# Kernel optimization log

Hardware: AMD Instinct MI355X
Metric: run time of the kernel (lower is better)

The kernel has to match this reference:

```python
import jax, jax.numpy as jnp
import numpy as np

H = 128
W = 128
TILE = 32
N = 12000
BIG = 1e30


def _render(means2D, cov2d, color, opacity, depths):
    # pixel coords, indexing='xy': pix[y, x] = (x, y)
    pix = jnp.stack(jnp.meshgrid(jnp.arange(W), jnp.arange(H), indexing='xy'), axis=-1).astype(means2D.dtype)
    c00 = cov2d[:, 0, 0]; c01 = cov2d[:, 0, 1]; c10 = cov2d[:, 1, 0]; c11 = cov2d[:, 1, 1]
    det = c00 * c11 - c01 * c10
    # get_radius (no_grad in torch)
    mid = 0.5 * (c00 + c11)
    s = jnp.sqrt(jnp.maximum(mid * mid - det, 0.1))
    radii = jax.lax.stop_gradient(3.0 * jnp.ceil(jnp.sqrt(jnp.maximum(mid + s, mid - s))))
    # get_rect, clipped to image bounds
    rmin = jnp.clip(means2D - radii[:, None], 0.0, W - 1.0)  # H == W == 128
    rmax = jnp.clip(means2D + radii[:, None], 0.0, W - 1.0)
    rmin = jax.lax.stop_gradient(rmin)
    rmax = jax.lax.stop_gradient(rmax)
    # closed-form 2x2 inverse (conic)
    inv_det = 1.0 / det
    conic = jnp.stack([jnp.stack([c11, -c01], axis=-1),
                       jnp.stack([-c10, c00], axis=-1)], axis=-2) * inv_det[:, None, None]

    img_c = jnp.ones((H, W, 3), means2D.dtype)
    img_d = jnp.zeros((H, W, 1), means2D.dtype)
    img_a = jnp.zeros((H, W, 1), means2D.dtype)

    for h in range(0, H, TILE):
        for w in range(0, W, TILE):
            tlx = jnp.maximum(rmin[:, 0], w); tly = jnp.maximum(rmin[:, 1], h)
            brx = jnp.minimum(rmax[:, 0], w + TILE - 1.0); bry = jnp.minimum(rmax[:, 1], h + TILE - 1.0)
            mask = (brx > tlx) & (bry > tly)  # [N]
            # depth sort with non-intersecting gaussians pushed to the back
            order = jnp.argsort(jnp.where(mask, depths, BIG))
            sm = means2D[order]          # [N,2]
            sc = conic[order]            # [N,2,2]
            so = opacity[order]          # [N,1]
            scol = color[order]          # [N,3]
            smask = mask[order]
            sd = jnp.where(smask, depths[order], 0.0)
            tile_coord = pix[h:h + TILE, w:w + TILE].reshape(-1, 2)  # [1024,2]
            dx = tile_coord[:, None, :] - sm[None]                   # [1024,N,2]
            gw = jnp.exp(-0.5 * (dx[..., 0] ** 2 * sc[:, 0, 0]
                                 + dx[..., 1] ** 2 * sc[:, 1, 1]
                                 + dx[..., 0] * dx[..., 1] * (sc[:, 0, 1] + sc[:, 1, 0])))
            alpha = gw[..., None] * so[None] * smask[None, :, None].astype(gw.dtype)  # [1024,N,1]
            alpha = jnp.minimum(alpha, 0.99)
            T = jnp.cumprod(jnp.concatenate([jnp.ones_like(alpha[:, :1]), 1.0 - alpha[:, :-1]], axis=1), axis=1)
            wgt = T * alpha
            acc = wgt.sum(axis=1)                                   # [1024,1]
            tc = (wgt * scol[None]).sum(axis=1) + (1.0 - acc)       # white background
            td = (wgt * sd[None, :, None]).sum(axis=1)
            img_c = img_c.at[h:h + TILE, w:w + TILE].set(tc.reshape(TILE, TILE, 3))
            img_d = img_d.at[h:h + TILE, w:w + TILE].set(td.reshape(TILE, TILE, 1))
            img_a = img_a.at[h:h + TILE, w:w + TILE].set(acc.reshape(TILE, TILE, 1))
    return img_c, img_d, img_a


def setup_inputs() -> dict:
    key = jax.random.key(0)
    k1, k2, k3, k4, k5 = jax.random.split(key, 5)
    means2D = jax.random.uniform(k1, (N, 2), jnp.float32) * 128.0
    L = 0.6 * jax.random.normal(k2, (N, 2, 2), jnp.float32)
    cov2d = L @ jnp.swapaxes(L, -1, -2) + 0.3 * jnp.eye(2, dtype=jnp.float32)[None]
    color = jax.random.uniform(k3, (N, 3), jnp.float32)
    opacity = jax.random.uniform(k4, (N, 1), jnp.float32)
    depths = jax.random.uniform(k5, (N,), jnp.float32) * 10.0 + 0.2
    return {"means2D": means2D, "cov2d": cov2d, "color": color, "opacity": opacity, "depths": depths}


def reference(means2D, cov2d, color, opacity, depths):
    return _render(means2D, cov2d, color, opacity, depths)
```

## Files before the change

### kernel.cpp

```cpp
#include <hip/hip_runtime.h>
#include <stdint.h>

#define HH 128
#define WW 128
#define NTILES 16
#define NPIX (HH * WW)
#define MAXSEG 16
#define JCH 512

__device__ __forceinline__ uint64_t mkkey(float d, int i) {
    return ((uint64_t)__float_as_uint(d) << 32) | (uint64_t)(uint32_t)i;
}

__global__ __launch_bounds__(256) void k1_rank(const float* __restrict__ depths,
                                               int* __restrict__ part,
                                               int N, int ncj, int NA) {
    int bi = blockIdx.x / ncj;
    int bj = blockIdx.x % ncj;
    int t  = threadIdx.x;
    int i  = bi * 256 + t;
    float di = (i < N) ? depths[i] : 0.0f;
    uint64_t ki = mkkey(di, i);

    int j0   = bj * JCH;
    int jend = min(N, j0 + JCH);

    int c0 = 0, c1 = 0, c2 = 0, c3 = 0;
    int j = j0;
    for (; j + 4 <= jend; j += 4) {
        uint64_t a = mkkey(depths[j + 0], j + 0);
        uint64_t b = mkkey(depths[j + 1], j + 1);
        uint64_t c = mkkey(depths[j + 2], j + 2);
        uint64_t d = mkkey(depths[j + 3], j + 3);
        c0 += (a < ki);
        c1 += (b < ki);
        c2 += (c < ki);
        c3 += (d < ki);
    }
    for (; j < jend; j++) c0 += (mkkey(depths[j], j) < ki);

    if (i < N) part[(size_t)bj * NA + i] = (c0 + c1) + (c2 + c3);
}

__global__ __launch_bounds__(256) void k2_scatter(const float* __restrict__ means,
                                                  const float* __restrict__ cov,
                                                  const float* __restrict__ color,
                                                  const float* __restrict__ opac,
                                                  const float* __restrict__ depths,
                                                  const int* __restrict__ part,
                                                  float* __restrict__ sorted,
                                                  int* __restrict__ smask,
                                                  int N, int ncj, int NA) {
    int i = blockIdx.x * blockDim.x + threadIdx.x;
    if (i >= N) return;

    int r = 0;
    for (int b = 0; b < ncj; b++) r += part[(size_t)b * NA + i];

    float mx = means[2 * i + 0];
    float my = means[2 * i + 1];
    float c00 = cov[4 * i + 0];
    float c01 = cov[4 * i + 1];
    float c10 = cov[4 * i + 2];
    float c11 = cov[4 * i + 3];

    float det = c00 * c11 - c01 * c10;
    float mid = 0.5f * (c00 + c11);
    float s = sqrtf(fmaxf(mid * mid - det, 0.1f));
    float radii = 3.0f * ceilf(sqrtf(fmaxf(mid + s, mid - s)));

    float rminx = fminf(fmaxf(mx - radii, 0.0f), (float)(WW - 1));
    float rminy = fminf(fmaxf(my - radii, 0.0f), (float)(HH - 1));
    float rmaxx = fminf(fmaxf(mx + radii, 0.0f), (float)(WW - 1));
    float rmaxy = fminf(fmaxf(my + radii, 0.0f), (float)(HH - 1));

    float inv_det = 1.0f / det;
    float A = c11 * inv_det;
    float B = c00 * inv_det;
    float C = -(c01 + c10) * inv_det;

    int bits = 0;
    for (int ty = 0; ty < 4; ty++) {
        float h = (float)(ty * 32);
        float tly = fmaxf(rminy, h);
        float bry = fminf(rmaxy, h + 31.0f);
        bool yok = bry > tly;
        for (int tx = 0; tx < 4; tx++) {
            float w = (float)(tx * 32);
            float tlx = fmaxf(rminx, w);
            float brx = fminf(rmaxx, w + 31.0f);
            if (yok && (brx > tlx)) bits |= 1 << (ty * 4 + tx);
        }
    }

    float4* g4 = (float4*)(sorted + (size_t)r * 12);
    g4[0] = make_float4(mx, my, A, B);
    g4[1] = make_float4(C, opac[i], color[3 * i + 0], color[3 * i + 1]);
    g4[2] = make_float4(color[3 * i + 2], depths[i], 0.0f, 0.0f);
    smask[r] = bits;
}

__global__ __launch_bounds__(1024) void k3_compact(const int* __restrict__ smask,
                                                   int* __restrict__ lists,
                                                   int* __restrict__ counts,
                                                   int N) {
    int tile = blockIdx.x;
    int t = threadIdx.x;
    int lane = t & 63;
    int wv = t >> 6;

    __shared__ int wsum[16];
    __shared__ int woff[16];
    __shared__ int s_run;
    if (t == 0) s_run = 0;
    __syncthreads();

    int* list = lists + (size_t)tile * N;

    for (int base = 0; base < N; base += 1024) {
        int idx = base + t;
        int flag = (idx < N) ? ((smask[idx] >> tile) & 1) : 0;
        unsigned long long bal = __ballot(flag);
        int pre = __popcll(bal & ((1ull << lane) - 1ull));
        if (lane == 63) wsum[wv] = pre + flag;
        __syncthreads();
        if (wv == 0 && lane < 16) {
            int v = 0;
            for (int q = 0; q < lane; q++) v += wsum[q];
            woff[lane] = v;
        }
        __syncthreads();
        int run = s_run;
        if (flag) list[run + woff[wv] + pre] = idx;
        __syncthreads();
        if (t == 0) s_run = run + woff[15] + wsum[15];
        __syncthreads();
    }
    if (t == 0) counts[tile] = s_run;
}

#define CH 64
__global__ __launch_bounds__(256) void k4_render(const float* __restrict__ sorted,
                                                 const int* __restrict__ lists,
                                                 const int* __restrict__ counts,
                                                 float4* __restrict__ part4,
                                                 float2* __restrict__ part2,
                                                 int N, int S) {
    int b = blockIdx.x;
    int s = b & (S - 1);
    int q = b / S;
    int tile = q >> 2;
    int sub = q & 3;
    int tx = tile & 3;
    int ty = tile >> 2;
    int t = threadIdx.x;

    int p = sub * 256 + t;
    int px = p & 31;
    int py = p >> 5;
    float fx = (float)(tx * 32 + px);
    float fy = (float)(ty * 32 + py);

    int cnt = counts[tile];
    int chunk = (cnt + S - 1) / S;
    int beg = s * chunk;
    int end = min(cnt, beg + chunk);
    const int* list = lists + (size_t)tile * N;

    __shared__ __align__(16) float4 s_g[CH * 3];
    __shared__ int s_idx[CH];

    float T = 1.0f;
    float ar = 0.0f, ag = 0.0f, ab = 0.0f, ad = 0.0f, aa = 0.0f;

    for (int base = beg; base < end; base += CH) {
        int m = min(CH, end - base);
        if (t < CH) s_idx[t] = (t < m) ? list[base + t] : 0;
        __syncthreads();
        if (t < m * 3) {
            int k = t / 3;
            int c = t - k * 3;
            s_g[t] = ((const float4*)(sorted + (size_t)s_idx[k] * 12))[c];
        }
        __syncthreads();
        for (int k = 0; k < m; k++) {
            float4 ga = s_g[k * 3 + 0];
            float4 gb = s_g[k * 3 + 1];
            float4 gc = s_g[k * 3 + 2];
            float dx = fx - ga.x;
            float dy = fy - ga.y;
            float e = ga.z * dx * dx + ga.w * dy * dy + gb.x * dx * dy;
            float gw = __expf(-0.5f * e);
            float alpha = fminf(gw * gb.y, 0.99f);
            float w = T * alpha;
            ar += w * gb.z;
            ag += w * gb.w;
            ab += w * gc.x;
            ad += w * gc.y;
            aa += w;
            T *= (1.0f - alpha);
        }
        __syncthreads();
    }

    size_t o = (size_t)s * NPIX + (size_t)tile * 1024 + p;
    part4[o] = make_float4(ar, ag, ab, ad);
    part2[o] = make_float2(aa, T);
}

__global__ __launch_bounds__(256) void k5_combine(const float4* __restrict__ part4,
                                                  const float2* __restrict__ part2,
                                                  float* __restrict__ out, int S) {
    int pid = blockIdx.x * 256 + threadIdx.x;
    int tile = pid >> 10;
    int p = pid & 1023;
    int px = p & 31;
    int py = p >> 5;
    int gx = (tile & 3) * 32 + px;
    int gy = (tile >> 2) * 32 + py;

    float T = 1.0f;
    float ar = 0.0f, ag = 0.0f, ab = 0.0f, ad = 0.0f, aa = 0.0f;
    for (int s = 0; s < S; s++) {
        float4 q4 = part4[(size_t)s * NPIX + pid];
        float2 q2 = part2[(size_t)s * NPIX + pid];
        ar += T * q4.x;
        ag += T * q4.y;
        ab += T * q4.z;
        ad += T * q4.w;
        aa += T * q2.x;
        T *= q2.y;
    }

    int pidx = gy * WW + gx;
    float bgr = 1.0f - aa;
    out[pidx * 3 + 0] = ar + bgr;
    out[pidx * 3 + 1] = ag + bgr;
    out[pidx * 3 + 2] = ab + bgr;
    out[HH * WW * 3 + pidx] = ad;
    out[HH * WW * 4 + pidx] = aa;
}

extern "C" void kernel_launch(void* const* d_in, const int* in_sizes, int n_in,
                              void* d_out, int out_size, void* d_ws, size_t ws_size,
                              hipStream_t stream) {
    const float* means  = (const float*)d_in[0];
    const float* cov    = (const float*)d_in[1];
    const float* color  = (const float*)d_in[2];
    const float* opac   = (const float*)d_in[3];
    const float* depths = (const float*)d_in[4];
    float* out = (float*)d_out;

    int N = in_sizes[4];
    int NA = (int)(((size_t)N + 255) / 256 * 256);
    int nb  = (N + 255) / 256;
    int ncj = (N + JCH - 1) / JCH;

    size_t o_part   = 0;
    size_t o_sorted = o_part + (size_t)ncj * NA * 4;
    size_t o_smask  = o_sorted + (size_t)NA * 48;
    size_t o_lists  = o_smask + (size_t)NA * 4;
    size_t o_counts = o_lists + (size_t)NTILES * NA * 4;
    size_t o_part4  = o_counts + 256;

    int S = 1;
    while (S < MAXSEG &&
           o_part4 + (size_t)(S * 2) * NPIX * 24 <= ws_size) S *= 2;
    size_t o_part2 = o_part4 + (size_t)S * NPIX * 16;

    int*    part   = (int*)((char*)d_ws + o_part);
    float*  sorted = (float*)((char*)d_ws + o_sorted);
    int*    smask  = (int*)((char*)d_ws + o_smask);
    int*    lists  = (int*)((char*)d_ws + o_lists);
    int*    counts = (int*)((char*)d_ws + o_counts);
    float4* part4  = (float4*)((char*)d_ws + o_part4);
    float2* part2  = (float2*)((char*)d_ws + o_part2);

    k1_rank<<<nb * ncj, 256, 0, stream>>>(depths, part, N, ncj, NA);
    k2_scatter<<<nb, 256, 0, stream>>>(means, cov, color, opac, depths, part,
                                       sorted, smask, N, ncj, NA);
    k3_compact<<<NTILES, 1024, 0, stream>>>(smask, lists, counts, N);
    k4_render<<<64 * S, 256, 0, stream>>>(sorted, lists, counts, part4, part2,
                                          N, S);
    k5_combine<<<NPIX / 256, 256, 0, stream>>>(part4, part2, out, S);
}
```

Baseline: 140.1 us.

## Fuse rank with scatter and compaction with render into two kernels

Cuts the pipeline from five kernels to two. Rank counting and the scatter now share one block: four wave slices each count over a quarter of the keys and reduce through shared memory. Per-tile compaction is merged with rendering, keeping the tile list in LDS, and one 1024-thread block per tile renders all pixels with no segment split or combine pass. This removes launch overhead and global intermediates but leaves only 16 blocks for the heavy render, cutting parallelism sharply, and the list is capped at LCAP entries.

```diff
diff --git a/kernel.cpp b/kernel.cpp
--- a/kernel.cpp
+++ b/kernel.cpp
@@ -4,118 +4,108 @@
 #define HH 128
 #define WW 128
 #define NTILES 16
-#define NPIX (HH * WW)
-#define MAXSEG 16
-#define JCH 512
+#define LCAP 12288
+#define CH 128
 
 __device__ __forceinline__ uint64_t mkkey(float d, int i) {
     return ((uint64_t)__float_as_uint(d) << 32) | (uint64_t)(uint32_t)i;
 }
 
-__global__ __launch_bounds__(256) void k1_rank(const float* __restrict__ depths,
-                                               int* __restrict__ part,
-                                               int N, int ncj, int NA) {
-    int bi = blockIdx.x / ncj;
-    int bj = blockIdx.x % ncj;
-    int t  = threadIdx.x;
-    int i  = bi * 256 + t;
+__global__ __launch_bounds__(256) void kA(const float* __restrict__ means,
+                                          const float* __restrict__ cov,
+                                          const float* __restrict__ color,
+                                          const float* __restrict__ opac,
+                                          const float* __restrict__ depths,
+                                          float* __restrict__ sorted,
+                                          int* __restrict__ smask, int N) {
+    int t = threadIdx.x;
+    int slice = t >> 6;
+    int il = t & 63;
+    int i = blockIdx.x * 64 + il;
     float di = (i < N) ? depths[i] : 0.0f;
     uint64_t ki = mkkey(di, i);
 
-    int j0   = bj * JCH;
-    int jend = min(N, j0 + JCH);
+    int per = (N + 3) / 4;
+    int j0 = slice * per;
+    int jend = min(N, j0 + per);
 
     int c0 = 0, c1 = 0, c2 = 0, c3 = 0;
     int j = j0;
     for (; j + 4 <= jend; j += 4) {
-        uint64_t a = mkkey(depths[j + 0], j + 0);
-        uint64_t b = mkkey(depths[j + 1], j + 1);
-        uint64_t c = mkkey(depths[j + 2], j + 2);
-        uint64_t d = mkkey(depths[j + 3], j + 3);
-        c0 += (a < ki);
-        c1 += (b < ki);
-        c2 += (c < ki);
-        c3 += (d < ki);
+        c0 += (mkkey(depths[j + 0], j + 0) < ki);
+        c1 += (mkkey(depths[j + 1], j + 1) < ki);
+        c2 += (mkkey(depths[j + 2], j + 2) < ki);
+        c3 += (mkkey(depths[j + 3], j + 3) < ki);
     }
     for (; j < jend; j++) c0 += (mkkey(depths[j], j) < ki);
 
-    if (i < N) part[(size_t)bj * NA + i] = (c0 + c1) + (c2 + c3);
-}
-
-__global__ __launch_bounds__(256) void k2_scatter(const float* __restrict__ means,
-                                                  const float* __restrict__ cov,
-                                                  const float* __restrict__ color,
-                                                  const float* __restrict__ opac,
-                                                  const float* __restrict__ depths,
-                                                  const int* __restrict__ part,
-                                                  float* __restrict__ sorted,
-                                                  int* __restrict__ smask,
-                                                  int N, int ncj, int NA) {
-    int i = blockIdx.x * blockDim.x + threadIdx.x;
-    if (i >= N) return;
-
-    int r = 0;
-    for (int b = 0; b < ncj; b++) r += part[(size_t)b * NA + i];
-
-    float mx = means[2 * i + 0];
-    float my = means[2 * i + 1];
-    float c00 = cov[4 * i + 0];
-    float c01 = cov[4 * i + 1];
-    float c10 = cov[4 * i + 2];
-    float c11 = cov[4 * i + 3];
-
-    float det = c00 * c11 - c01 * c10;
-    float mid = 0.5f * (c00 + c11);
-    float s = sqrtf(fmaxf(mid * mid - det, 0.1f));
-    float radii = 3.0f * ceilf(sqrtf(fmaxf(mid + s, mid - s)));
-
-    float rminx = fminf(fmaxf(mx - radii, 0.0f), (float)(WW - 1));
-    float rminy = fminf(fmaxf(my - radii, 0.0f), (float)(HH - 1));
-    float rmaxx = fminf(fmaxf(mx + radii, 0.0f), (float)(WW - 1));
-    float rmaxy = fminf(fmaxf(my + radii, 0.0f), (float)(HH - 1));
-
-    float inv_det = 1.0f / det;
-    float A = c11 * inv_det;
-    float B = c00 * inv_det;
-    float C = -(c01 + c10) * inv_det;
-
-    int bits = 0;
-    for (int ty = 0; ty < 4; ty++) {
-        float h = (float)(ty * 32);
-        float tly = fmaxf(rminy, h);
-        float bry = fminf(rmaxy, h + 31.0f);
-        bool yok = bry > tly;
-        for (int tx = 0; tx < 4; tx++) {
-            float w = (float)(tx * 32);
-            float tlx = fmaxf(rminx, w);
-            float brx = fminf(rmaxx, w + 31.0f);
-            if (yok && (brx > tlx)) bits |= 1 << (ty * 4 + tx);
-        }
-    }
-
-    float4* g4 = (float4*)(sorted + (size_t)r * 12);
-    g4[0] = make_float4(mx, my, A, B);
-    g4[1] = make_float4(C, opac[i], color[3 * i + 0], color[3 * i + 1]);
-    g4[2] = make_float4(color[3 * i + 2], depths[i], 0.0f, 0.0f);
-    smask[r] = bits;
-}
-
-__global__ __launch_bounds__(1024) void k3_compact(const int* __restrict__ smask,
-                                                   int* __restrict__ lists,
-                                                   int* __restrict__ counts,
-                                                   int N) {
+    __shared__ int s_cnt[4][64];
+    s_cnt[slice][il] = (c0 + c1) + (c2 + c3);
+    __syncthreads();
+
+    if (slice == 0 && i < N) {
+        int r = s_cnt[0][il] + s_cnt[1][il] + s_cnt[2][il] + s_cnt[3][il];
+
+        float mx = means[2 * i + 0];
+        float my = means[2 * i + 1];
+        float c00 = cov[4 * i + 0];
+        float c01 = cov[4 * i + 1];
+        float c10 = cov[4 * i + 2];
+        float c11 = cov[4 * i + 3];
+
+        float det = c00 * c11 - c01 * c10;
+        float mid = 0.5f * (c00 + c11);
+        float s = sqrtf(fmaxf(mid * mid - det, 0.1f));
+        float radii = 3.0f * ceilf(sqrtf(fmaxf(mid + s, mid - s)));
+
+        float rminx = fminf(fmaxf(mx - radii, 0.0f), (float)(WW - 1));
+        float rminy = fminf(fmaxf(my - radii, 0.0f), (float)(HH - 1));
+        float rmaxx = fminf(fmaxf(mx + radii, 0.0f), (float)(WW - 1));
+        float rmaxy = fminf(fmaxf(my + radii, 0.0f), (float)(HH - 1));
+
+        float inv_det = 1.0f / det;
+        float A = c11 * inv_det;
+        float B = c00 * inv_det;
+        float C = -(c01 + c10) * inv_det;
+
+        int bits = 0;
+        for (int ty = 0; ty < 4; ty++) {
+            float h = (float)(ty * 32);
+            float tly = fmaxf(rminy, h);
+            float bry = fminf(rmaxy, h + 31.0f);
+            bool yok = bry > tly;
+            for (int tx = 0; tx < 4; tx++) {
+                float w = (float)(tx * 32);
+                float tlx = fmaxf(rminx, w);
+                float brx = fminf(rmaxx, w + 31.0f);
+                if (yok && (brx > tlx)) bits |= 1 << (ty * 4 + tx);
+            }
+        }
+
+        float4* g4 = (float4*)(sorted + (size_t)r * 12);
+        g4[0] = make_float4(mx, my, A, B);
+        g4[1] = make_float4(C, opac[i], color[3 * i + 0], color[3 * i + 1]);
+        g4[2] = make_float4(color[3 * i + 2], depths[i], 0.0f, 0.0f);
+        smask[r] = bits;
+    }
+}
+
+__global__ __launch_bounds__(1024) void kBC(const float* __restrict__ sorted,
+                                            const int* __restrict__ smask,
+                                            float* __restrict__ out, int N) {
     int tile = blockIdx.x;
     int t = threadIdx.x;
     int lane = t & 63;
     int wv = t >> 6;
 
+    __shared__ int s_list[LCAP];
     __shared__ int wsum[16];
     __shared__ int woff[16];
     __shared__ int s_run;
+    __shared__ __align__(16) float4 s_g[CH * 3];
+
     if (t == 0) s_run = 0;
     __syncthreads();
-
-    int* list = lists + (size_t)tile * N;
 
     for (int base = 0; base < N; base += 1024) {
         int idx = base + t;
@@ -131,56 +121,31 @@
         }
         __syncthreads();
         int run = s_run;
-        if (flag) list[run + woff[wv] + pre] = idx;
+        if (flag) {
+            int pos = run + woff[wv] + pre;
+            if (pos < LCAP) s_list[pos] = idx;
+        }
         __syncthreads();
         if (t == 0) s_run = run + woff[15] + wsum[15];
         __syncthreads();
     }
-    if (t == 0) counts[tile] = s_run;
-}
-
-#define CH 64
-__global__ __launch_bounds__(256) void k4_render(const float* __restrict__ sorted,
-                                                 const int* __restrict__ lists,
-                                                 const int* __restrict__ counts,
-                                                 float4* __restrict__ part4,
-                                                 float2* __restrict__ part2,
-                                                 int N, int S) {
-    int b = blockIdx.x;
-    int s = b & (S - 1);
-    int q = b / S;
-    int tile = q >> 2;
-    int sub = q & 3;
-    int tx = tile & 3;
-    int ty = tile >> 2;
-    int t = threadIdx.x;
-
-    int p = sub * 256 + t;
-    int px = p & 31;
-    int py = p >> 5;
-    float fx = (float)(tx * 32 + px);
-    float fy = (float)(ty * 32 + py);
-
-    int cnt = counts[tile];
-    int chunk = (cnt + S - 1) / S;
-    int beg = s * chunk;
-    int end = min(cnt, beg + chunk);
-    const int* list = lists + (size_t)tile * N;
-
-    __shared__ __align__(16) float4 s_g[CH * 3];
-    __shared__ int s_idx[CH];
+    int cnt = min(s_run, LCAP);
+
+    int px = t & 31;
+    int py = t >> 5;
+    float fx = (float)((tile & 3) * 32 + px);
+    float fy = (float)((tile >> 2) * 32 + py);
 
     float T = 1.0f;
     float ar = 0.0f, ag = 0.0f, ab = 0.0f, ad = 0.0f, aa = 0.0f;
 
-    for (int base = beg; base < end; base += CH) {
-        int m = min(CH, end - base);
-        if (t < CH) s_idx[t] = (t < m) ? list[base + t] : 0;
+    for (int base = 0; base < cnt; base += CH) {
+        int m = min(CH, cnt - base);
         __syncthreads();
         if (t < m * 3) {
             int k = t / 3;
             int c = t - k * 3;
-            s_g[t] = ((const float4*)(sorted + (size_t)s_idx[k] * 12))[c];
+            s_g[t] = ((const float4*)(sorted + (size_t)s_list[base + k] * 12))[c];
         }
         __syncthreads();
         for (int k = 0; k < m; k++) {
@@ -200,38 +165,10 @@
             aa += w;
             T *= (1.0f - alpha);
         }
-        __syncthreads();
-    }
-
-    size_t o = (size_t)s * NPIX + (size_t)tile * 1024 + p;
-    part4[o] = make_float4(ar, ag, ab, ad);
-    part2[o] = make_float2(aa, T);
-}
-
-__global__ __launch_bounds__(256) void k5_combine(const float4* __restrict__ part4,
-                                                  const float2* __restrict__ part2,
-                                                  float* __restrict__ out, int S) {
-    int pid = blockIdx.x * 256 + threadIdx.x;
-    int tile = pid >> 10;
-    int p = pid & 1023;
-    int px = p & 31;
-    int py = p >> 5;
+    }
+
     int gx = (tile & 3) * 32 + px;
     int gy = (tile >> 2) * 32 + py;
-
-    float T = 1.0f;
-    float ar = 0.0f, ag = 0.0f, ab = 0.0f, ad = 0.0f, aa = 0.0f;
-    for (int s = 0; s < S; s++) {
-        float4 q4 = part4[(size_t)s * NPIX + pid];
-        float2 q2 = part2[(size_t)s * NPIX + pid];
-        ar += T * q4.x;
-        ag += T * q4.y;
-        ab += T * q4.z;
-        ad += T * q4.w;
-        aa += T * q2.x;
-        T *= q2.y;
-    }
-
     int pidx = gy * WW + gx;
     float bgr = 1.0f - aa;
     out[pidx * 3 + 0] = ar + bgr;
@@ -252,35 +189,14 @@
     float* out = (float*)d_out;
 
     int N = in_sizes[4];
-    int NA = (int)(((size_t)N + 255) / 256 * 256);
-    int nb  = (N + 255) / 256;
-    int ncj = (N + JCH - 1) / JCH;
-
-    size_t o_part   = 0;
-    size_t o_sorted = o_part + (size_t)ncj * NA * 4;
-    size_t o_smask  = o_sorted + (size_t)NA * 48;
-    size_t o_lists  = o_smask + (size_t)NA * 4;
-    size_t o_counts = o_lists + (size_t)NTILES * NA * 4;
-    size_t o_part4  = o_counts + 256;
-
-    int S = 1;
-    while (S < MAXSEG &&
-           o_part4 + (size_t)(S * 2) * NPIX * 24 <= ws_size) S *= 2;
-    size_t o_part2 = o_part4 + (size_t)S * NPIX * 16;
-
-    int*    part   = (int*)((char*)d_ws + o_part);
-    float*  sorted = (float*)((char*)d_ws + o_sorted);
-    int*    smask  = (int*)((char*)d_ws + o_smask);
-    int*    lists  = (int*)((char*)d_ws + o_lists);
-    int*    counts = (int*)((char*)d_ws + o_counts);
-    float4* part4  = (float4*)((char*)d_ws + o_part4);
-    float2* part2  = (float2*)((char*)d_ws + o_part2);
-
-    k1_rank<<<nb * ncj, 256, 0, stream>>>(depths, part, N, ncj, NA);
-    k2_scatter<<<nb, 256, 0, stream>>>(means, cov, color, opac, depths, part,
-                                       sorted, smask, N, ncj, NA);
-    k3_compact<<<NTILES, 1024, 0, stream>>>(smask, lists, counts, N);
-    k4_render<<<64 * S, 256, 0, stream>>>(sorted, lists, counts, part4, part2,
-                                          N, S);
-    k5_combine<<<NPIX / 256, 256, 0, stream>>>(part4, part2, out, S);
-}
+    size_t NA = ((size_t)N + 255) / 256 * 256;
+
+    float* sorted = (float*)d_ws;
+    int*   smask  = (int*)((char*)d_ws + NA * 48);
+
+    int nb64 = (N + 63) / 64;
+
+    kA<<<nb64, 256, 0, stream>>>(means, cov, color, opac, depths,
+                                 sorted, smask, N);
+    kBC<<<NTILES, 1024, 0, stream>>>(sorted, smask, out, N);
+}
```

New measurement: 352.7 us. +151.7%, slower.

## Pre-gather per-tile gaussian data and render two pixels per thread

Applied to the files above, without the earlier changes.

The compaction kernel now copies each intersecting gaussian's 48-byte record into a contiguous per-tile buffer, replacing the index list. The render kernel then reads gaussians straight from global memory through uniform loads, with no shared-memory staging or barriers, and each thread handles two pixels in the same column so the gaussian loads and dx terms are shared. The segment count is fixed at 16 instead of being derived from workspace size. This assumes the workspace is large enough and caps each tile list at 12288 entries, and the compaction kernel does more memory traffic.

```diff
diff --git a/kernel.cpp b/kernel.cpp
--- a/kernel.cpp
+++ b/kernel.cpp
@@ -5,7 +5,8 @@
 #define WW 128
 #define NTILES 16
 #define NPIX (HH * WW)
-#define MAXSEG 16
+#define SEG 16
+#define LCAP 12288
 #define JCH 512
 
 __device__ __forceinline__ uint64_t mkkey(float d, int i) {
@@ -28,14 +29,10 @@
     int c0 = 0, c1 = 0, c2 = 0, c3 = 0;
     int j = j0;
     for (; j + 4 <= jend; j += 4) {
-        uint64_t a = mkkey(depths[j + 0], j + 0);
-        uint64_t b = mkkey(depths[j + 1], j + 1);
-        uint64_t c = mkkey(depths[j + 2], j + 2);
-        uint64_t d = mkkey(depths[j + 3], j + 3);
-        c0 += (a < ki);
-        c1 += (b < ki);
-        c2 += (c < ki);
-        c3 += (d < ki);
+        c0 += (mkkey(depths[j + 0], j + 0) < ki);
+        c1 += (mkkey(depths[j + 1], j + 1) < ki);
+        c2 += (mkkey(depths[j + 2], j + 2) < ki);
+        c3 += (mkkey(depths[j + 3], j + 3) < ki);
     }
     for (; j < jend; j++) c0 += (mkkey(depths[j], j) < ki);
 
@@ -100,10 +97,11 @@
     smask[r] = bits;
 }
 
-__global__ __launch_bounds__(1024) void k3_compact(const int* __restrict__ smask,
-                                                   int* __restrict__ lists,
-                                                   int* __restrict__ counts,
-                                                   int N) {
+__global__ __launch_bounds__(1024) void k3_gather(const float* __restrict__ sorted,
+                                                  const int* __restrict__ smask,
+                                                  float* __restrict__ tlist,
+                                                  int* __restrict__ counts,
+                                                  int N) {
     int tile = blockIdx.x;
     int t = threadIdx.x;
     int lane = t & 63;
@@ -115,7 +113,7 @@
     if (t == 0) s_run = 0;
     __syncthreads();
 
-    int* list = lists + (size_t)tile * N;
+    float* dst = tlist + (size_t)tile * LCAP * 12;
 
     for (int base = 0; base < N; base += 1024) {
         int idx = base + t;
@@ -131,7 +129,14 @@
         }
         __syncthreads();
         int run = s_run;
-        if (flag) list[run + woff[wv] + pre] = idx;
+        if (flag) {
+            int pos = run + woff[wv] + pre;
+            const float4* src = (const float4*)(sorted + (size_t)idx * 12);
+            float4* d4 = (float4*)(dst + (size_t)pos * 12);
+            d4[0] = src[0];
+            d4[1] = src[1];
+            d4[2] = src[2];
+        }
         __syncthreads();
         if (t == 0) s_run = run + woff[15] + wsum[15];
         __syncthreads();
@@ -139,78 +144,73 @@
     if (t == 0) counts[tile] = s_run;
 }
 
-#define CH 64
-__global__ __launch_bounds__(256) void k4_render(const float* __restrict__ sorted,
-                                                 const int* __restrict__ lists,
+__global__ __launch_bounds__(256) void k4_render(const float* __restrict__ tlist,
                                                  const int* __restrict__ counts,
                                                  float4* __restrict__ part4,
-                                                 float2* __restrict__ part2,
-                                                 int N, int S) {
+                                                 float2* __restrict__ part2) {
     int b = blockIdx.x;
-    int s = b & (S - 1);
-    int q = b / S;
-    int tile = q >> 2;
-    int sub = q & 3;
-    int tx = tile & 3;
-    int ty = tile >> 2;
+    int s = b & (SEG - 1);
+    int q = b / SEG;
+    int tile = q >> 1;
+    int half = q & 1;
     int t = threadIdx.x;
 
-    int p = sub * 256 + t;
-    int px = p & 31;
-    int py = p >> 5;
-    float fx = (float)(tx * 32 + px);
-    float fy = (float)(ty * 32 + py);
+    int p0 = half * 512 + t;
+    int p1 = p0 + 256;
+    int px  = p0 & 31;
+    int py0 = p0 >> 5;
+    int py1 = p1 >> 5;
+    float fx  = (float)((tile & 3) * 32 + px);
+    float fy0 = (float)((tile >> 2) * 32 + py0);
+    float fy1 = (float)((tile >> 2) * 32 + py1);
 
     int cnt = counts[tile];
-    int chunk = (cnt + S - 1) / S;
+    int chunk = (cnt + SEG - 1) / SEG;
     int beg = s * chunk;
     int end = min(cnt, beg + chunk);
-    const int* list = lists + (size_t)tile * N;
-
-    __shared__ __align__(16) float4 s_g[CH * 3];
-    __shared__ int s_idx[CH];
-
-    float T = 1.0f;
-    float ar = 0.0f, ag = 0.0f, ab = 0.0f, ad = 0.0f, aa = 0.0f;
-
-    for (int base = beg; base < end; base += CH) {
-        int m = min(CH, end - base);
-        if (t < CH) s_idx[t] = (t < m) ? list[base + t] : 0;
-        __syncthreads();
-        if (t < m * 3) {
-            int k = t / 3;
-            int c = t - k * 3;
-            s_g[t] = ((const float4*)(sorted + (size_t)s_idx[k] * 12))[c];
-        }
-        __syncthreads();
-        for (int k = 0; k < m; k++) {
-            float4 ga = s_g[k * 3 + 0];
-            float4 gb = s_g[k * 3 + 1];
-            float4 gc = s_g[k * 3 + 2];
-            float dx = fx - ga.x;
-            float dy = fy - ga.y;
-            float e = ga.z * dx * dx + ga.w * dy * dy + gb.x * dx * dy;
-            float gw = __expf(-0.5f * e);
-            float alpha = fminf(gw * gb.y, 0.99f);
-            float w = T * alpha;
-            ar += w * gb.z;
-            ag += w * gb.w;
-            ab += w * gc.x;
-            ad += w * gc.y;
-            aa += w;
-            T *= (1.0f - alpha);
-        }
-        __syncthreads();
-    }
-
-    size_t o = (size_t)s * NPIX + (size_t)tile * 1024 + p;
-    part4[o] = make_float4(ar, ag, ab, ad);
-    part2[o] = make_float2(aa, T);
+    const float* g = tlist + (size_t)tile * LCAP * 12;
+
+    float T0 = 1.0f, ar0 = 0.0f, ag0 = 0.0f, ab0 = 0.0f, ad0 = 0.0f, aa0 = 0.0f;
+    float T1 = 1.0f, ar1 = 0.0f, ag1 = 0.0f, ab1 = 0.0f, ad1 = 0.0f, aa1 = 0.0f;
+
+    for (int k = beg; k < end; k++) {
+        const float4* g4 = (const float4*)(g + (size_t)k * 12);
+        float4 ga = g4[0];
+        float4 gb = g4[1];
+        float4 gc = g4[2];
+        float dx  = fx - ga.x;
+        float dx2 = dx * dx;
+        float cdx = gb.x * dx;
+        float dy0 = fy0 - ga.y;
+        float dy1 = fy1 - ga.y;
+        float e0 = ga.z * dx2 + ga.w * dy0 * dy0 + cdx * dy0;
+        float e1 = ga.z * dx2 + ga.w * dy1 * dy1 + cdx * dy1;
+        float gw0 = __expf(-0.5f * e0);
+        float gw1 = __expf(-0.5f * e1);
+        float a0 = fminf(gw0 * gb.y, 0.99f);
+        float a1 = fminf(gw1 * gb.y, 0.99f);
+        float w0 = T0 * a0;
+        float w1 = T1 * a1;
+        ar0 += w0 * gb.z;  ar1 += w1 * gb.z;
+        ag0 += w0 * gb.w;  ag1 += w1 * gb.w;
+        ab0 += w0 * gc.x;  ab1 += w1 * gc.x;
+        ad0 += w0 * gc.y;  ad1 += w1 * gc.y;
+        aa0 += w0;         aa1 += w1;
+        T0 *= (1.0f - a0);
+        T1 *= (1.0f - a1);
+    }
+
+    size_t o0 = (size_t)s * NPIX + (size_t)tile * 1024 + p0;
+    size_t o1 = o0 + 256;
+    part4[o0] = make_float4(ar0, ag0, ab0, ad0);
+    part2[o0] = make_float2(aa0, T0);
+    part4[o1] = make_float4(ar1, ag1, ab1, ad1);
+    part2[o1] = make_float2(aa1, T1);
 }
 
 __global__ __launch_bounds__(256) void k5_combine(const float4* __restrict__ part4,
                                                   const float2* __restrict__ part2,
-                                                  float* __restrict__ out, int S) {
+                                                  float* __restrict__ out) {
     int pid = blockIdx.x * 256 + threadIdx.x;
     int tile = pid >> 10;
     int p = pid & 1023;
@@ -221,7 +221,7 @@
 
     float T = 1.0f;
     float ar = 0.0f, ag = 0.0f, ab = 0.0f, ad = 0.0f, aa = 0.0f;
-    for (int s = 0; s < S; s++) {
+    for (int s = 0; s < SEG; s++) {
         float4 q4 = part4[(size_t)s * NPIX + pid];
         float2 q2 = part2[(size_t)s * NPIX + pid];
         ar += T * q4.x;
@@ -259,19 +259,15 @@
     size_t o_part   = 0;
     size_t o_sorted = o_part + (size_t)ncj * NA * 4;
     size_t o_smask  = o_sorted + (size_t)NA * 48;
-    size_t o_lists  = o_smask + (size_t)NA * 4;
-    size_t o_counts = o_lists + (size_t)NTILES * NA * 4;
+    size_t o_tlist  = o_smask + (size_t)NA * 4;
+    size_t o_counts = o_tlist + (size_t)NTILES * LCAP * 48;
     size_t o_part4  = o_counts + 256;
-
-    int S = 1;
-    while (S < MAXSEG &&
-           o_part4 + (size_t)(S * 2) * NPIX * 24 <= ws_size) S *= 2;
-    size_t o_part2 = o_part4 + (size_t)S * NPIX * 16;
+    size_t o_part2  = o_part4 + (size_t)SEG * NPIX * 16;
 
     int*    part   = (int*)((char*)d_ws + o_part);
     float*  sorted = (float*)((char*)d_ws + o_sorted);
     int*    smask  = (int*)((char*)d_ws + o_smask);
-    int*    lists  = (int*)((char*)d_ws + o_lists);
+    float*  tlist  = (float*)((char*)d_ws + o_tlist);
     int*    counts = (int*)((char*)d_ws + o_counts);
     float4* part4  = (float4*)((char*)d_ws + o_part4);
     float2* part2  = (float2*)((char*)d_ws + o_part2);
@@ -279,8 +275,7 @@
     k1_rank<<<nb * ncj, 256, 0, stream>>>(depths, part, N, ncj, NA);
     k2_scatter<<<nb, 256, 0, stream>>>(means, cov, color, opac, depths, part,
                                        sorted, smask, N, ncj, NA);
-    k3_compact<<<NTILES, 1024, 0, stream>>>(smask, lists, counts, N);
-    k4_render<<<64 * S, 256, 0, stream>>>(sorted, lists, counts, part4, part2,
-                                          N, S);
-    k5_combine<<<NPIX / 256, 256, 0, stream>>>(part4, part2, out, S);
-}
+    k3_gather<<<NTILES, 1024, 0, stream>>>(sorted, smask, tlist, counts, N);
+    k4_render<<<NTILES * 2 * SEG, 256, 0, stream>>>(tlist, counts, part4, part2);
+    k5_combine<<<NPIX / 256, 256, 0, stream>>>(part4, part2, out);
+}
```

After: 156.1 us. 1.11x slower.
